# Kernel tuning notes

Hardware: AMD Instinct MI355X
Metric: run time of the kernel (lower is better)

The kernel has to match this reference:

```python
import jax, jax.numpy as jnp
import numpy as np
from jax import lax

K = 32            # module k
T = 1             # train_ensemble -> times_sampled
LARGE = 1e10      # LARGE_NUMBER in source
NEG = -1e30       # finite stand-in for -inf (keeps grads NaN-free)


def prefix_logesp(theta, k):
    """Prefix log elementary symmetric polynomials of weights w_i = exp(theta_i).
    theta: (BE, N). Returns F of shape (N+1, BE, k+1) with F[i, b, j] = log e_j(w_1..w_i).
    """
    BE = theta.shape[0]
    init = jnp.concatenate([jnp.zeros((BE, 1), theta.dtype),
                            jnp.full((BE, k), NEG, theta.dtype)], axis=1)

    def step(E, th):
        shifted = jnp.concatenate([jnp.full((BE, 1), NEG, E.dtype), E[:, :-1]], axis=1) + th[:, None]
        Enew = jnp.logaddexp(E, shifted)
        return Enew, Enew

    _, Es = lax.scan(step, init, theta.T)            # Es: (N, BE, k+1)
    return jnp.concatenate([init[None], Es], axis=0)  # (N+1, BE, k+1)


def simple_core(flat, k, times_sampled, key):
    """SIMPLE k-subset layer: exact marginals (log_pr) + conditional-Poisson sampling,
    with straight-through gradient through the marginals (matches the .detach() trick).
    flat: (BE, N) logits. Returns samples (T, BE, N) and marginals (BE, N).
    """
    BE, N = flat.shape
    F = prefix_logesp(flat, k)                       # prefix ESPs, (N+1, BE, k+1)
    B = prefix_logesp(flat[:, ::-1], k)[::-1]        # suffix ESPs: B[i] = ESP of items i..N-1

    # marginal p_i = w_i * e_{k-1}(w \ i) / e_k(w)
    comb = F[:N, :, :k] + B[1:, :, :k][:, :, ::-1]   # (N, BE, k): j + (k-1-j) split
    log_ekm1 = jax.scipy.special.logsumexp(comb, axis=2)  # (N, BE)
    logZ = F[N, :, k]                                # (BE,) log e_k of all weights
    logp = flat.T + log_ekm1 - logZ[None]            # (N, BE)
    marginals = jnp.exp(logp).T                      # (BE, N)

    # exact sequential sampling from the k-subset (conditional Poisson) distribution
    U = jax.random.uniform(key, (N, times_sampled, BE))
    be = jnp.arange(BE)[None, :]

    def samp_step(r, xs):
        th_i, Bi, Bip1, u = xs                       # th_i: (BE,), Bi/Bip1: (BE, k+1), u: (T, BE)
        rm1 = jnp.maximum(r - 1, 0)
        logq = th_i[None, :] + Bip1[be, rm1] - Bi[be, r]
        incl = (u < jnp.exp(jnp.minimum(logq, 0.0))) & (r > 0)
        return r - incl.astype(r.dtype), incl.astype(flat.dtype)

    r0 = jnp.full((times_sampled, BE), k, dtype=jnp.int32)
    _, bits = lax.scan(samp_step, r0, (flat.T, B[:-1], B[1:], U))  # bits: (N, T, BE)
    samples = jnp.transpose(bits, (1, 2, 0))         # (T, BE, N) hard k-hot
    # straight-through: (samples - marginals).detach() + marginals
    samples = lax.stop_gradient(samples - marginals[None]) + marginals[None]
    return samples, marginals


def setup_inputs() -> dict:
    key = jax.random.key(0)
    scores = jax.random.normal(key, (128, 4096, 2), dtype=jnp.float32)
    return {"scores": scores}


def reference(scores):
    bsz, Nmax, ens = scores.shape
    # policy == 'edge_candid'
    flat = jnp.transpose(scores, (0, 2, 1)).reshape(bsz * ens, Nmax)
    target = Nmax
    k = min(K, Nmax)
    N = 2 ** int(np.ceil(np.log2(target)))
    if N > target:  # pad to power of 2 with -LARGE (no-op for Nmax=4096)
        pad = jnp.full((flat.shape[0], N - target), -LARGE, flat.dtype)
        flat = jnp.concatenate([flat, pad], axis=1)
    # logits_activation is None -> pass through
    samples, marginals = simple_core(flat, k, T, jax.random.key(42))
    samples = samples[..., :target]
    marginals = marginals[:, :target]
    new_mask = samples.reshape(T, bsz, ens, Nmax).transpose(0, 1, 3, 2)      # (T, B, Nmax, E)
    new_marginals = marginals.reshape(bsz, ens, Nmax).transpose(0, 2, 1)     # (B, Nmax, E)
    return new_mask, new_marginals
```

## Files before the change

### kernel.cpp

```cpp
#include <hip/hip_runtime.h>
#include <stdint.h>

#pragma clang fp contract(off)

#define BE_C     256
#define N_C      4096
#define K_C      32
#define NEG_C    (-1e30f)
#define OUT_HALF 1048576

__device__ __forceinline__ float xla_exp(float x) {
  const float exp_hi = 88.3762626647950f;
  const float exp_lo = -88.3762626647949f;
  const float log2ef = 1.44269504088896341f;
  const float c1 = 0.693359375f;
  const float c2 = -2.12194440e-4f;
  const float p0 = 1.9875691500E-4f;
  const float p1 = 1.3981999507E-3f;
  const float p2 = 8.3334519073E-3f;
  const float p3 = 4.1665795894E-2f;
  const float p4 = 1.6666665459E-1f;
  const float p5 = 5.0000001201E-1f;
  float xc = fminf(fmaxf(x, exp_lo), exp_hi);
  float fx = floorf(xc * log2ef + 0.5f);
  float tmp = c1 * fx;
  float z = c2 * fx;
  float xx = xc - tmp;
  xx = xx - z;
  z = xx * xx;
  float y = xx * p0 + p1;
  y = y * xx + p2;
  y = y * xx + p3;
  y = y * xx + p4;
  y = y * xx + p5;
  y = y * z + xx;
  y = y + 1.0f;
  int ei = (int)fx;
  float s = __int_as_float((ei + 127) << 23);
  return fmaxf(y * s, x);
}

__device__ __forceinline__ float xla_log(float xin) {
  const float sqrthf = 0.707106781186547524f;
  const float p0 = 7.0376836292E-2f;
  const float p1 = -1.1514610310E-1f;
  const float p2 = 1.1676998740E-1f;
  const float p3 = -1.2420140846E-1f;
  const float p4 = 1.4249322787E-1f;
  const float p5 = -1.6668057665E-1f;
  const float p6 = 2.0000714765E-1f;
  const float p7 = -2.4999993993E-1f;
  const float p8 = 3.3333331174E-1f;
  const float q1 = -2.12194440e-4f;
  const float q2 = 0.693359375f;
  float x = fmaxf(xin, 1.17549435e-38f);
  unsigned ub = __float_as_uint(x);
  int emm0 = (int)(ub >> 23) - 0x7f;
  float e = 1.0f + (float)emm0;
  x = __uint_as_float((ub & 0x007fffffu) | 0x3f000000u);
  bool mlt = x < sqrthf;
  float tmp = mlt ? x : 0.0f;
  x = x - 1.0f;
  e = e - (mlt ? 1.0f : 0.0f);
  x = x + tmp;
  float x2 = x * x;
  float x3 = x2 * x;
  float y  = x * p0 + p1;
  float y1 = x * p3 + p4;
  float y2 = x * p6 + p7;
  y  = y * x + p2;
  y1 = y1 * x + p5;
  y2 = y2 * x + p8;
  y = y * x3 + y1;
  y = y * x3 + y2;
  y = y * x3;
  y1 = q1 * e;
  float t2 = 0.5f * x2;
  y = y + y1;
  x = x - t2;
  y2 = q2 * e;
  x = x + y;
  x = x + y2;
  return x;
}

__device__ __forceinline__ float xla_log1p(float x) {
  float ax = fabsf(x);
  float fsmall = ((-0.5f * x) + 1.0f) * x;
  float flarge = xla_log(x + 1.0f);
  return (ax < 1e-4f) ? fsmall : flarge;
}

__device__ __forceinline__ float xla_logaddexp(float a, float b) {
  float mx = fmaxf(a, b);
  float d = a - b;
  float e = xla_exp(-fabsf(d));
  return mx + xla_log1p(e);
}

__device__ __forceinline__ float fast_la(float a, float b) {
  float mx = fmaxf(a, b);
  float d = a - b;
  float e = __expf(-fabsf(d));
  return mx + __logf(1.0f + e);
}

__device__ __forceinline__ float dpp_shr1(float x, float fill) {
  int r = __builtin_amdgcn_update_dpp(__float_as_int(fill), __float_as_int(x),
                                      0x138, 0xF, 0xF, false);
  return __int_as_float(r);
}

__device__ __forceinline__ unsigned rotl_(unsigned v, int r) {
  return (v << r) | (v >> (32 - r));
}

__device__ __forceinline__ void threefry_0_42(unsigned c0, unsigned c1,
                                              unsigned* o0, unsigned* o1) {
  const unsigned ks0 = 0u, ks1 = 42u, ks2 = 0x1BD11BDAu ^ 0u ^ 42u;
  unsigned x0 = c0 + ks0, x1 = c1 + ks1;
  x0 += x1; x1 = rotl_(x1, 13); x1 ^= x0;
  x0 += x1; x1 = rotl_(x1, 15); x1 ^= x0;
  x0 += x1; x1 = rotl_(x1, 26); x1 ^= x0;
  x0 += x1; x1 = rotl_(x1, 6);  x1 ^= x0;
  x0 += ks1; x1 += ks2 + 1u;
  x0 += x1; x1 = rotl_(x1, 17); x1 ^= x0;
  x0 += x1; x1 = rotl_(x1, 29); x1 ^= x0;
  x0 += x1; x1 = rotl_(x1, 16); x1 ^= x0;
  x0 += x1; x1 = rotl_(x1, 24); x1 ^= x0;
  x0 += ks2; x1 += ks0 + 2u;
  x0 += x1; x1 = rotl_(x1, 13); x1 ^= x0;
  x0 += x1; x1 = rotl_(x1, 15); x1 ^= x0;
  x0 += x1; x1 = rotl_(x1, 26); x1 ^= x0;
  x0 += x1; x1 = rotl_(x1, 6);  x1 ^= x0;
  x0 += ks0; x1 += ks1 + 3u;
  x0 += x1; x1 = rotl_(x1, 17); x1 ^= x0;
  x0 += x1; x1 = rotl_(x1, 29); x1 ^= x0;
  x0 += x1; x1 = rotl_(x1, 16); x1 ^= x0;
  x0 += x1; x1 = rotl_(x1, 24); x1 ^= x0;
  x0 += ks1; x1 += ks2 + 4u;
  x0 += x1; x1 = rotl_(x1, 13); x1 ^= x0;
  x0 += x1; x1 = rotl_(x1, 15); x1 ^= x0;
  x0 += x1; x1 = rotl_(x1, 26); x1 ^= x0;
  x0 += x1; x1 = rotl_(x1, 6);  x1 ^= x0;
  x0 += ks2; x1 += ks0 + 5u;
  *o0 = x0; *o1 = x1;
}

__device__ __forceinline__ float u01_from_idx(unsigned idx) {
  unsigned b0, b1;
  threefry_0_42(0u, idx, &b0, &b1);
  unsigned bits = b0 ^ b1;
  unsigned fb = (bits >> 9) | 0x3f800000u;
  return __uint_as_float(fb) - 1.0f;
}

__device__ __forceinline__ int sw_idx(int row, int col) {
  return row * 32 + ((col + row) & 31);
}

__global__ __launch_bounds__(256)
void EdgeSIMPLEBatched_39298950758997_kernel(const float* __restrict__ scores,
                                             float* __restrict__ out) {
  __shared__ float th_lds[N_C];
  __shared__ float chkB[64 * 32];
  __shared__ float chkF[63 * 32];
  __shared__ float logZ_s;
  __shared__ int   prodCnt;
  __shared__ int   consCnt[2];
  __shared__ union OvT {
    struct {
      float u[N_C];
      float ring[2 * 32 * 64];
    } p1;
    float wbuf[4][64 * 32];
  } ov;

  const int t = threadIdx.x;
  const int w = t >> 6;
  const int lane = t & 63;
  const int b = blockIdx.x;
  const int bi = b >> 1, ens = b & 1;
  const float* srow = scores + bi * (N_C * 2) + ens;

  for (int idx = t; idx < N_C; idx += 256) {
    th_lds[idx] = srow[idx * 2];
    ov.p1.u[idx] = u01_from_idx((unsigned)(idx * BE_C + b));
  }
  if (t == 0) { prodCnt = 0; consCnt[0] = 0; consCnt[1] = 0; }
  __syncthreads();

  if (w == 0) {
    float E = (lane == 0) ? 0.0f : NEG_C;
    if (lane < 32) chkB[63 * 32 + lane] = E;
    float th = th_lds[N_C - 1];
#pragma unroll 1
    for (int bb = 0; bb < 128; ++bb) {
      if (bb >= 2) {
        volatile int* cc = &consCnt[bb & 1];
        while (*cc < bb - 1) __builtin_amdgcn_s_sleep(1);
      }
      float* ring = ov.p1.ring + (bb & 1) * (32 * 64);
#pragma unroll 2
      for (int l = 0; l < 32; ++l) {
        const int i = N_C - 1 - (bb * 32 + l);
        const int ip = (i > 0) ? i - 1 : 0;
        float th_nx = th_lds[ip];
        float Em1 = dpp_shr1(E, NEG_C);
        float sh = Em1 + th;
        float Enew = xla_logaddexp(E, sh);
        float logq = (th + Em1) - Enew;
        ring[l * 64 + lane] = logq;
        E = Enew;
        if ((i & 63) == 0 && i > 0 && lane < 32) chkB[((i >> 6) - 1) * 32 + lane] = E;
        th = th_nx;
      }
      __threadfence_block();
      if (lane == 0) *(volatile int*)&prodCnt = bb + 1;
    }
    if (lane == 32) logZ_s = E;
  } else if (w == 1) {
    float F = (lane == 0) ? 0.0f : NEG_C;
    float th = th_lds[0];
#pragma unroll 2
    for (int i = 0; i < N_C; ++i) {
      float th_nx = th_lds[(i + 1 < N_C) ? i + 1 : i];
      if ((i & 63) == 0 && i > 0 && lane < 32) chkF[((i >> 6) - 1) * 32 + lane] = F;
      float Fm1 = dpp_shr1(F, NEG_C);
      F = fast_la(F, Fm1 + th);
      th = th_nx;
    }
  } else {
    const int par = w - 2;
#pragma unroll 1
    for (int bb = par; bb < 128; bb += 2) {
      { volatile int* pc = &prodCnt;
        while (*pc < bb + 1) __builtin_amdgcn_s_sleep(1); }
      float* ring = ov.p1.ring + (bb & 1) * (32 * 64);
#pragma unroll 2
      for (int l = 0; l < 32; ++l) {
        const int i = N_C - 1 - (bb * 32 + l);
        float logq = ring[l * 64 + lane];
        float u = ov.p1.u[i];
        float q = xla_exp(fminf(logq, 0.0f));
        unsigned long long bal = __ballot(u < q);
        if (lane == 0)
          out[bi * (N_C * 2) + i * 2 + ens] = __uint_as_float((unsigned)(bal >> 1));
      }
      __threadfence_block();
      if (lane == 0) *(volatile int*)&consCnt[par] = bb + 1;
    }
  }
  __syncthreads();

  const float logZ = logZ_s;
  float* wb = ov.wbuf[w];
  for (int c = w; c < 64; c += 4) {
    float E2 = chkB[c * 32 + (lane & 31)];
    if (lane < 32) wb[sw_idx(63, lane)] = E2;
#pragma unroll 1
    for (int ii = 63; ii >= 1; --ii) {
      float th = th_lds[c * 64 + ii];
      float Em1 = dpp_shr1(E2, NEG_C);
      E2 = fast_la(E2, Em1 + th);
      if (lane < 32) wb[sw_idx(ii - 1, lane)] = E2;
    }
    float F2;
    if (c == 0) F2 = (lane == 0) ? 0.0f : NEG_C;
    else        F2 = (lane < 32) ? chkF[(c - 1) * 32 + lane] : NEG_C;
    float th = th_lds[c * 64];
#pragma unroll 2
    for (int ii = 0; ii < 64; ++ii) {
      float th_nx = th_lds[c * 64 + ((ii + 1 < 64) ? ii + 1 : ii)];
      float bbv = wb[sw_idx(ii, (31 - lane) & 31)];
      float comb = F2 + bbv;
      if (lane < 32) wb[sw_idx(ii, lane)] = comb;
      float Fm1 = dpp_shr1(F2, NEG_C);
      F2 = fast_la(F2, Fm1 + th);
      th = th_nx;
    }
    __threadfence_block();
    float cb[32];
#pragma unroll
    for (int jj = 0; jj < 32; ++jj) cb[jj] = wb[sw_idx(lane, jj)];
    float amax = cb[0];
#pragma unroll
    for (int jj = 1; jj < 32; ++jj) amax = fmaxf(amax, cb[jj]);
    float ss = 0.0f;
#pragma unroll
    for (int jj = 0; jj < 32; ++jj) ss += __expf(cb[jj] - amax);
    float thi = th_lds[c * 64 + lane];
    float m = __expf((thi + (__logf(ss) + amax)) - logZ);
    out[OUT_HALF + bi * (N_C * 2) + (c * 64 + lane) * 2 + ens] = m;
  }
  __syncthreads();

  if (w == 0) {
    int r = K_C;
    for (int c = 0; c < 64; ++c) {
      const int i = c * 64 + lane;
      const int oidx = bi * (N_C * 2) + i * 2 + ens;
      float mval = out[OUT_HALF + oidx];
      unsigned mymask = __float_as_uint(out[oidx]);
      unsigned incl = 0u;
#pragma unroll 8
      for (int ii = 0; ii < 64; ++ii) {
        unsigned mm = (unsigned)__builtin_amdgcn_readlane((int)mymask, ii);
        unsigned bit = (mm >> ((unsigned)(r - 1) & 31u)) & 1u;
        bit = (r > 0) ? bit : 0u;
        if (lane == ii) incl = bit;
        r -= (int)bit;
      }
      float sval = incl ? ((1.0f - mval) + mval) : 0.0f;
      out[oidx] = sval;
    }
  }
}

extern "C" void kernel_launch(void* const* d_in, const int* in_sizes, int n_in,
                              void* d_out, int out_size, void* d_ws, size_t ws_size,
                              hipStream_t stream) {
  (void)in_sizes; (void)n_in; (void)d_ws; (void)ws_size; (void)out_size;
  const float* scores = (const float*)d_in[0];
  float* out = (float*)d_out;
  EdgeSIMPLEBatched_39298950758997_kernel<<<dim3(BE_C), dim3(256), 0, stream>>>(scores, out);
}
```

Measured before the change: 1.235 ms.

## Fuse sampling probability test into backward scan and transpose inclusion bitmasks

The two consumer waves and the producer/consumer ring buffer with spin-wait counters are removed. Wave 0 now computes the acceptance test itself, using readlane-broadcast theta and uniform values, and packs per-lane 32-bit masks over item groups instead of ballots over lanes. The final sequential walk reads the mask lane indexed by the remaining count r, and the exp/log clamps that cannot trigger on the known value ranges are dropped. This removes LDS handoff and sync overhead but lengthens the serial critical path of wave 0 by adding an exp per step.

```diff
diff --git a/kernel.cpp b/kernel.cpp
--- a/kernel.cpp
+++ b/kernel.cpp
@@ -9,8 +9,7 @@
 #define NEG_C    (-1e30f)
 #define OUT_HALF 1048576
 
-__device__ __forceinline__ float xla_exp(float x) {
-  const float exp_hi = 88.3762626647950f;
+__device__ __forceinline__ float xla_exp_neg(float x) {
   const float exp_lo = -88.3762626647949f;
   const float log2ef = 1.44269504088896341f;
   const float c1 = 0.693359375f;
@@ -21,7 +20,7 @@
   const float p3 = 4.1665795894E-2f;
   const float p4 = 1.6666665459E-1f;
   const float p5 = 5.0000001201E-1f;
-  float xc = fminf(fmaxf(x, exp_lo), exp_hi);
+  float xc = fmaxf(x, exp_lo);
   float fx = floorf(xc * log2ef + 0.5f);
   float tmp = c1 * fx;
   float z = c2 * fx;
@@ -37,10 +36,10 @@
   y = y + 1.0f;
   int ei = (int)fx;
   float s = __int_as_float((ei + 127) << 23);
-  return fmaxf(y * s, x);
-}
-
-__device__ __forceinline__ float xla_log(float xin) {
+  return y * s;
+}
+
+__device__ __forceinline__ float xla_log_12(float xin) {
   const float sqrthf = 0.707106781186547524f;
   const float p0 = 7.0376836292E-2f;
   const float p1 = -1.1514610310E-1f;
@@ -53,7 +52,7 @@
   const float p8 = 3.3333331174E-1f;
   const float q1 = -2.12194440e-4f;
   const float q2 = 0.693359375f;
-  float x = fmaxf(xin, 1.17549435e-38f);
+  float x = xin;
   unsigned ub = __float_as_uint(x);
   int emm0 = (int)(ub >> 23) - 0x7f;
   float e = 1.0f + (float)emm0;
@@ -84,18 +83,17 @@
   return x;
 }
 
-__device__ __forceinline__ float xla_log1p(float x) {
-  float ax = fabsf(x);
+__device__ __forceinline__ float xla_log1p_01(float x) {
   float fsmall = ((-0.5f * x) + 1.0f) * x;
-  float flarge = xla_log(x + 1.0f);
-  return (ax < 1e-4f) ? fsmall : flarge;
+  float flarge = xla_log_12(x + 1.0f);
+  return (fabsf(x) < 1e-4f) ? fsmall : flarge;
 }
 
 __device__ __forceinline__ float xla_logaddexp(float a, float b) {
   float mx = fmaxf(a, b);
   float d = a - b;
-  float e = xla_exp(-fabsf(d));
-  return mx + xla_log1p(e);
+  float e = xla_exp_neg(-fabsf(d));
+  return mx + xla_log1p_01(e);
 }
 
 __device__ __forceinline__ float fast_la(float a, float b) {
@@ -109,6 +107,10 @@
   int r = __builtin_amdgcn_update_dpp(__float_as_int(fill), __float_as_int(x),
                                       0x138, 0xF, 0xF, false);
   return __int_as_float(r);
+}
+
+__device__ __forceinline__ float readlane_f(float v, int l) {
+  return __int_as_float(__builtin_amdgcn_readlane(__float_as_int(v), l));
 }
 
 __device__ __forceinline__ unsigned rotl_(unsigned v, int r) {
@@ -166,13 +168,8 @@
   __shared__ float chkB[64 * 32];
   __shared__ float chkF[63 * 32];
   __shared__ float logZ_s;
-  __shared__ int   prodCnt;
-  __shared__ int   consCnt[2];
   __shared__ union OvT {
-    struct {
-      float u[N_C];
-      float ring[2 * 32 * 64];
-    } p1;
+    float u[N_C];
     float wbuf[4][64 * 32];
   } ov;
 
@@ -182,41 +179,45 @@
   const int b = blockIdx.x;
   const int bi = b >> 1, ens = b & 1;
   const float* srow = scores + bi * (N_C * 2) + ens;
+  const int obase = bi * (N_C * 2) + ens;
 
   for (int idx = t; idx < N_C; idx += 256) {
     th_lds[idx] = srow[idx * 2];
-    ov.p1.u[idx] = u01_from_idx((unsigned)(idx * BE_C + b));
+    ov.u[idx] = u01_from_idx((unsigned)(idx * BE_C + b));
   }
-  if (t == 0) { prodCnt = 0; consCnt[0] = 0; consCnt[1] = 0; }
   __syncthreads();
 
   if (w == 0) {
     float E = (lane == 0) ? 0.0f : NEG_C;
     if (lane < 32) chkB[63 * 32 + lane] = E;
-    float th = th_lds[N_C - 1];
+    const int l31 = lane & 31;
+    float thb = th_lds[N_C - 1 - l31];
+    float ub  = ov.u[N_C - 1 - l31];
+    unsigned Wbits = 0u;
 #pragma unroll 1
-    for (int bb = 0; bb < 128; ++bb) {
-      if (bb >= 2) {
-        volatile int* cc = &consCnt[bb & 1];
-        while (*cc < bb - 1) __builtin_amdgcn_s_sleep(1);
-      }
-      float* ring = ov.p1.ring + (bb & 1) * (32 * 64);
-#pragma unroll 2
+    for (int g = 0; g < 128; ++g) {
+      const int nb = (g + 1 < 128) ? g + 1 : g;
+      float thb_n = th_lds[N_C - 1 - nb * 32 - l31];
+      float ub_n  = ov.u[N_C - 1 - nb * 32 - l31];
+#pragma unroll 4
       for (int l = 0; l < 32; ++l) {
-        const int i = N_C - 1 - (bb * 32 + l);
-        const int ip = (i > 0) ? i - 1 : 0;
-        float th_nx = th_lds[ip];
+        float th = readlane_f(thb, l);
+        float u  = readlane_f(ub, l);
         float Em1 = dpp_shr1(E, NEG_C);
         float sh = Em1 + th;
         float Enew = xla_logaddexp(E, sh);
         float logq = (th + Em1) - Enew;
-        ring[l * 64 + lane] = logq;
+        float q = xla_exp_neg(fminf(logq, 0.0f));
+        unsigned pb = (u < q) ? 1u : 0u;
+        Wbits |= pb << l;
         E = Enew;
-        if ((i & 63) == 0 && i > 0 && lane < 32) chkB[((i >> 6) - 1) * 32 + lane] = E;
-        th = th_nx;
       }
-      __threadfence_block();
-      if (lane == 0) *(volatile int*)&prodCnt = bb + 1;
+      if (lane >= 1 && lane <= 32)
+        out[obase + ((127 - g) * 32 + lane - 1) * 2] = __uint_as_float(Wbits);
+      Wbits = 0u;
+      if ((g & 1) == 1 && g < 127 && lane < 32)
+        chkB[(((127 - g) >> 1) - 1) * 32 + lane] = E;
+      thb = thb_n; ub = ub_n;
     }
     if (lane == 32) logZ_s = E;
   } else if (w == 1) {
@@ -229,26 +230,6 @@
       float Fm1 = dpp_shr1(F, NEG_C);
       F = fast_la(F, Fm1 + th);
       th = th_nx;
-    }
-  } else {
-    const int par = w - 2;
-#pragma unroll 1
-    for (int bb = par; bb < 128; bb += 2) {
-      { volatile int* pc = &prodCnt;
-        while (*pc < bb + 1) __builtin_amdgcn_s_sleep(1); }
-      float* ring = ov.p1.ring + (bb & 1) * (32 * 64);
-#pragma unroll 2
-      for (int l = 0; l < 32; ++l) {
-        const int i = N_C - 1 - (bb * 32 + l);
-        float logq = ring[l * 64 + lane];
-        float u = ov.p1.u[i];
-        float q = xla_exp(fminf(logq, 0.0f));
-        unsigned long long bal = __ballot(u < q);
-        if (lane == 0)
-          out[bi * (N_C * 2) + i * 2 + ens] = __uint_as_float((unsigned)(bal >> 1));
-      }
-      __threadfence_block();
-      if (lane == 0) *(volatile int*)&consCnt[par] = bb + 1;
     }
   }
   __syncthreads();
@@ -291,28 +272,37 @@
     for (int jj = 0; jj < 32; ++jj) ss += __expf(cb[jj] - amax);
     float thi = th_lds[c * 64 + lane];
     float m = __expf((thi + (__logf(ss) + amax)) - logZ);
-    out[OUT_HALF + bi * (N_C * 2) + (c * 64 + lane) * 2 + ens] = m;
+    out[OUT_HALF + obase + (c * 64 + lane) * 2] = m;
   }
   __syncthreads();
 
   if (w == 0) {
     int r = K_C;
-    for (int c = 0; c < 64; ++c) {
-      const int i = c * 64 + lane;
-      const int oidx = bi * (N_C * 2) + i * 2 + ens;
-      float mval = out[OUT_HALF + oidx];
-      unsigned mymask = __float_as_uint(out[oidx]);
-      unsigned incl = 0u;
+    const int l31 = lane & 31;
+    unsigned Wv = 0u;
+    if (lane >= 1 && lane <= 32)
+      Wv = __float_as_uint(out[obase + (lane - 1) * 2]);
+#pragma unroll 1
+    for (int g = 127; g >= 0; --g) {
+      unsigned Wn = 0u;
+      if (g > 0 && lane >= 1 && lane <= 32)
+        Wn = __float_as_uint(out[obase + ((128 - g) * 32 + lane - 1) * 2]);
+      const int i_l = N_C - 1 - 32 * g - l31;
+      float mval = out[OUT_HALF + obase + i_l * 2];
+      unsigned inclW = 0u;
 #pragma unroll 8
-      for (int ii = 0; ii < 64; ++ii) {
-        unsigned mm = (unsigned)__builtin_amdgcn_readlane((int)mymask, ii);
-        unsigned bit = (mm >> ((unsigned)(r - 1) & 31u)) & 1u;
-        bit = (r > 0) ? bit : 0u;
-        if (lane == ii) incl = bit;
+      for (int l = 31; l >= 0; --l) {
+        unsigned mm = (unsigned)__builtin_amdgcn_readlane((int)Wv, r);
+        unsigned bit = (mm >> l) & 1u;
+        inclW |= bit << l;
         r -= (int)bit;
       }
-      float sval = incl ? ((1.0f - mval) + mval) : 0.0f;
-      out[oidx] = sval;
+      if (lane < 32) {
+        unsigned incl = (inclW >> l31) & 1u;
+        float sval = incl ? ((1.0f - mval) + mval) : 0.0f;
+        out[obase + i_l * 2] = sval;
+      }
+      Wv = Wn;
     }
   }
 }
```

After: 1.216 ms. Within noise of the previous version (-1.5%).
